# Kernel tuning notes

Hardware: AMD Instinct MI355X
Metric: run time of the kernel (lower is better)

## Reference

```python
import jax, jax.numpy as jnp
import numpy as np

B = 65536
NC = 64          # coarse samples
NF = 128         # fine samples
NEAR, FAR = 2.0, 6.0


def setup_inputs() -> dict:
    key = jax.random.key(0)
    k1, k2, k3, k4, k5, k6 = jax.random.split(key, 6)
    ray_origin = jax.random.normal(k1, (B, 3), dtype=jnp.float32)
    ray_direction = jax.random.normal(k2, (B, 3), dtype=jnp.float32)
    # stratified linspace depths, as in the coarse branch of _sample_points_on_ray
    step = (FAR - NEAR) / (NC - 1)
    coarse_depth_values = jnp.broadcast_to(
        NEAR + jnp.arange(NC, dtype=jnp.float32) * step, (B, NC)
    )
    coarse_weights = jax.random.uniform(k3, (B, NC), dtype=jnp.float32)
    u = jax.random.uniform(k4, (B, NF), dtype=jnp.float32)
    raw_density = jax.random.uniform(k5, (B, NC + NF, 1), dtype=jnp.float32)
    raw_color = jax.random.uniform(k6, (B, NC + NF, 3), dtype=jnp.float32)
    return {
        "ray_origin": ray_origin,
        "ray_direction": ray_direction,
        "coarse_depth_values": coarse_depth_values,
        "coarse_weights": coarse_weights,
        "u": u,
        "raw_density": raw_density,
        "raw_color": raw_color,
    }


def _sample_pdf(bins, weights, u):
    """Inverse-CDF sampling. bins: [B, M+1], weights: [B, M], u: [B, N]."""
    M = weights.shape[1]
    weights = weights + 1e-5
    pdf = weights / jnp.sum(weights, axis=-1, keepdims=True)
    cdf = jnp.cumsum(pdf, axis=-1)                     # [B, M]
    cdf = jnp.concatenate([jnp.zeros_like(cdf[:, :1]), cdf], axis=-1)  # [B, M+1]
    # torch loop `above_inds += (u >= cdf[:, i])` for i in [0, M) ==
    # searchsorted(cdf[:, :M], u, side='right')
    above = jax.vmap(lambda c, uu: jnp.searchsorted(c, uu, side="right"))(
        cdf[:, :M], u
    )                                                  # [B, N], values in [1, M]
    below = jnp.clip(above - 1, 0, None)
    cdf_b = jnp.take_along_axis(cdf, below, axis=-1)
    cdf_a = jnp.take_along_axis(cdf, above, axis=-1)
    bins_b = jnp.take_along_axis(bins, below, axis=-1)
    bins_a = jnp.take_along_axis(bins, above, axis=-1)
    denom = cdf_a - cdf_b
    denom = jnp.where(denom < 1e-5, jnp.ones_like(denom), denom)
    t = (u - cdf_b) / denom
    return bins_b + t * (bins_a - bins_b)


def _composite(raw_density, raw_color, depth_values):
    # distances between consecutive samples, last one = 1e10
    dists = depth_values[..., 1:] - depth_values[..., :-1]
    dists = jnp.concatenate(
        [dists, jnp.full_like(dists[:, :1], 1e10)], axis=-1
    )
    alpha = 1.0 - jnp.exp(-raw_density[..., 0] * dists)          # [B, S]
    T = jnp.cumprod(1.0 - alpha + 1e-10, axis=-1)[:, :-1]
    T = jnp.concatenate([jnp.ones_like(T[:, :1]), T], axis=-1)
    weights = T * alpha                                           # [B, S]
    depth = jnp.sum(weights * depth_values, axis=-1, keepdims=True)
    color = jnp.sum(weights[..., None] * raw_color, axis=-2)      # [B, 3]
    return depth, color, weights


def reference(ray_origin, ray_direction, coarse_depth_values, coarse_weights,
              u, raw_density, raw_color):
    # fine branch of _sample_points_on_ray
    mids = 0.5 * (coarse_depth_values[..., 1:] + coarse_depth_values[..., :-1])
    w = coarse_weights[:, 1:-1]
    fine_depths = _sample_pdf(mids, w, u)                         # [B, NF]
    depth_values = jnp.sort(
        jnp.concatenate([coarse_depth_values, fine_depths], axis=-1), axis=-1
    )                                                             # [B, NC+NF]
    points_on_ray = (
        ray_origin[:, None, :]
        + ray_direction[:, None, :] * depth_values[..., None]
    )                                                             # [B, S, 3]
    depth, color_map, weights = _composite(raw_density, raw_color, depth_values)
    # forward of RenderRay returns the color map; points kept live via dummy use
    del points_on_ray, depth, weights
    return color_map
```

## Files before the change

### kernel.cpp

```cpp
#include <hip/hip_runtime.h>

#define NC 64
#define NF 128
#define NT 192
#define B_TOTAL 65536
#define RPB 4

#define NEAR_F 2.0f
#define STEP_F (4.0f / 63.0f)
#define INV_STEP (63.0f / 4.0f)

__global__ __launch_bounds__(256) void render_ray_kernel(
    const float* __restrict__ cw,
    const float* __restrict__ u_in,
    const float* __restrict__ dens,
    const float* __restrict__ col,
    float* __restrict__ out)
{
    const int wave = threadIdx.x >> 6;
    const int lane = threadIdx.x & 63;
    const int ray  = blockIdx.x * RPB + wave;

    __shared__ float s_cdf [RPB][64];
    __shared__ float s_m   [RPB][200];
    __shared__ int   s_hist[RPB][64];

    const float wraw = cw[(size_t)ray * NC + lane];
    float x = u_in[(size_t)ray * NF + lane];
    float y = u_in[(size_t)ray * NF + 64 + lane];

    const float wv = (lane >= 1 && lane <= 62) ? (wraw + 1e-5f) : 0.0f;
    float ssum = wv;
    #pragma unroll
    for (int off = 32; off; off >>= 1) ssum += __shfl_xor(ssum, off);
    const float pdf = __fdividef(wv, ssum);
    float scan = pdf;
    #pragma unroll
    for (int off = 1; off < 64; off <<= 1) {
        const float t = __shfl_up(scan, off);
        if (lane >= off) scan += t;
    }
    s_cdf[wave][lane]  = scan;
    s_hist[wave][lane] = 0;
    __syncthreads();

    #pragma unroll
    for (int k = 2; k <= 128; k <<= 1) {
        #pragma unroll
        for (int j = k >> 1; j > 0; j >>= 1) {
            if (j == 64) {
                const float mn = fminf(x, y);
                const float mx = fmaxf(x, y);
                x = mn; y = mx;
            } else {
                const bool lower = (lane & j) == 0;
                const bool ascx  = (k >= 128) ? true : ((lane & k) == 0);
                const bool ascy  = (k >= 128) ? true
                                 : ((k == 64) ? false : ((lane & k) == 0));
                const float px = __shfl_xor(x, j);
                const float py = __shfl_xor(y, j);
                x = (ascx == lower) ? fminf(x, px) : fmaxf(x, px);
                y = (ascy == lower) ? fminf(y, py) : fmaxf(y, py);
            }
        }
    }

    const float* __restrict__ cdfp = s_cdf[wave];
    auto sample = [&](float u) -> float {
        int l = 0, h = 62;
        while (l < h) {
            const int mid = (l + h) >> 1;
            if (cdfp[mid] <= u) l = mid + 1; else h = mid;
        }
        const int below = l - 1;
        const float cb = cdfp[below];
        const float ca = cdfp[l];
        float denom = ca - cb;
        if (denom < 1e-5f) denom = 1.0f;
        const float t = __fdividef(u - cb, denom);
        return NEAR_F + ((float)below + 0.5f + t) * STEP_F;
    };

    const float fx = sample(x);
    const float fy = sample(y);
    int gx = (int)floorf((fx - NEAR_F) * INV_STEP) + 1;
    int gy = (int)floorf((fy - NEAR_F) * INV_STEP) + 1;
    gx = min(max(gx, 1), 63);
    gy = min(max(gy, 1), 63);

    s_m[wave][lane + gx]      = fx;
    s_m[wave][lane + 64 + gy] = fy;
    atomicAdd(&s_hist[wave][gx], 1);
    atomicAdd(&s_hist[wave][gy], 1);
    __syncthreads();

    int hsum = s_hist[wave][lane];
    #pragma unroll
    for (int off = 1; off < 64; off <<= 1) {
        const int t = __shfl_up(hsum, off);
        if (lane >= off) hsum += t;
    }
    s_m[wave][lane + hsum] = NEAR_F + (float)lane * STEP_F;
    __syncthreads();

    const float* __restrict__ mp = s_m[wave];
    const int i0 = 3 * lane;
    const float m0 = mp[i0], m1 = mp[i0 + 1], m2 = mp[i0 + 2];
    const float m3 = mp[i0 + 3];
    const float d0 = m1 - m0;
    const float d1 = m2 - m1;
    const float d2 = (lane == 63) ? 1e10f : (m3 - m2);

    const float* __restrict__ dp = dens + (size_t)ray * NT + i0;
    const float a0 = 1.0f - __expf(-dp[0] * d0);
    const float a1 = 1.0f - __expf(-dp[1] * d1);
    const float a2 = 1.0f - __expf(-dp[2] * d2);
    const float f0 = 1.0f - a0 + 1e-10f;
    const float f1 = 1.0f - a1 + 1e-10f;
    const float f2 = 1.0f - a2 + 1e-10f;

    float scanp = f0 * f1 * f2;
    #pragma unroll
    for (int off = 1; off < 64; off <<= 1) {
        const float t = __shfl_up(scanp, off);
        if (lane >= off) scanp *= t;
    }
    float T0 = __shfl_up(scanp, 1);
    if (lane == 0) T0 = 1.0f;
    const float T1 = T0 * f0;
    const float T2 = T1 * f1;

    const float w0 = T0 * (1.0f - f0 + 1e-10f);
    const float w1 = T1 * (1.0f - f1 + 1e-10f);
    const float w2 = T2 * (1.0f - f2 + 1e-10f);

    const float* __restrict__ cp = col + (size_t)ray * NT * 3 + 3 * (size_t)i0;
    float ax = w0 * cp[0] + w1 * cp[3] + w2 * cp[6];
    float ay = w0 * cp[1] + w1 * cp[4] + w2 * cp[7];
    float az = w0 * cp[2] + w1 * cp[5] + w2 * cp[8];

    #pragma unroll
    for (int off = 32; off; off >>= 1) {
        ax += __shfl_xor(ax, off);
        ay += __shfl_xor(ay, off);
        az += __shfl_xor(az, off);
    }
    if (lane == 0) {
        out[(size_t)ray * 3 + 0] = ax;
        out[(size_t)ray * 3 + 1] = ay;
        out[(size_t)ray * 3 + 2] = az;
    }
}

extern "C" void kernel_launch(void* const* d_in, const int* in_sizes, int n_in,
                              void* d_out, int out_size, void* d_ws, size_t ws_size,
                              hipStream_t stream) {
    const float* cwts = (const float*)d_in[3];
    const float* u    = (const float*)d_in[4];
    const float* dens = (const float*)d_in[5];
    const float* col  = (const float*)d_in[6];
    float* out = (float*)d_out;

    dim3 grid(B_TOTAL / RPB);
    dim3 block(256);
    hipLaunchKernelGGL(render_ray_kernel, grid, block, 0, stream,
                       cwts, u, dens, col, out);
}
```

Measured before the change: 290.2 us.

## Prefetch density/color as float4 early, use wave barriers, 4 samples per lane

Issues vectorized float4 loads of density and color at kernel start so their latency overlaps the CDF, sort and search phases. The per-lane work is remapped to 4 samples on 48 lanes so those loads are aligned. Block-wide __syncthreads are replaced with wave barriers, since each wave works only on its own ray's shared memory. The three output components are now written by three lanes instead of one. This raises register pressure from holding the prefetched values and relies on wave-local LDS ordering being correct without a full barrier.

```diff
diff --git a/kernel.cpp b/kernel.cpp
--- a/kernel.cpp
+++ b/kernel.cpp
@@ -29,6 +29,15 @@
     float x = u_in[(size_t)ray * NF + lane];
     float y = u_in[(size_t)ray * NF + 64 + lane];
 
+    float4 dv = make_float4(0.f, 0.f, 0.f, 0.f);
+    float4 c0 = dv, c1 = dv, c2 = dv;
+    const int i0 = 4 * lane;
+    if (lane < 48) {
+        dv = *reinterpret_cast<const float4*>(dens + (size_t)ray * NT + i0);
+        const float4* cp4 = reinterpret_cast<const float4*>(col + (size_t)ray * NT * 3 + 3 * (size_t)i0);
+        c0 = cp4[0]; c1 = cp4[1]; c2 = cp4[2];
+    }
+
     const float wv = (lane >= 1 && lane <= 62) ? (wraw + 1e-5f) : 0.0f;
     float ssum = wv;
     #pragma unroll
@@ -42,7 +51,7 @@
     }
     s_cdf[wave][lane]  = scan;
     s_hist[wave][lane] = 0;
-    __syncthreads();
+    __builtin_amdgcn_wave_barrier();
 
     #pragma unroll
     for (int k = 2; k <= 128; k <<= 1) {
@@ -92,7 +101,7 @@
     s_m[wave][lane + 64 + gy] = fy;
     atomicAdd(&s_hist[wave][gx], 1);
     atomicAdd(&s_hist[wave][gy], 1);
-    __syncthreads();
+    __builtin_amdgcn_wave_barrier();
 
     int hsum = s_hist[wave][lane];
     #pragma unroll
@@ -101,25 +110,24 @@
         if (lane >= off) hsum += t;
     }
     s_m[wave][lane + hsum] = NEAR_F + (float)lane * STEP_F;
-    __syncthreads();
+    __builtin_amdgcn_wave_barrier();
 
     const float* __restrict__ mp = s_m[wave];
-    const int i0 = 3 * lane;
-    const float m0 = mp[i0], m1 = mp[i0 + 1], m2 = mp[i0 + 2];
-    const float m3 = mp[i0 + 3];
-    const float d0 = m1 - m0;
-    const float d1 = m2 - m1;
-    const float d2 = (lane == 63) ? 1e10f : (m3 - m2);
+    float f0 = 1.0f, f1 = 1.0f, f2 = 1.0f, f3 = 1.0f;
+    if (lane < 48) {
+        const float m0 = mp[i0], m1 = mp[i0 + 1], m2 = mp[i0 + 2], m3 = mp[i0 + 3];
+        const float m4 = mp[(lane == 47) ? 191 : (i0 + 4)];
+        const float d0 = m1 - m0;
+        const float d1 = m2 - m1;
+        const float d2 = m3 - m2;
+        const float d3 = (lane == 47) ? 1e10f : (m4 - m3);
+        f0 = 1.0f - (1.0f - __expf(-dv.x * d0)) + 1e-10f;
+        f1 = 1.0f - (1.0f - __expf(-dv.y * d1)) + 1e-10f;
+        f2 = 1.0f - (1.0f - __expf(-dv.z * d2)) + 1e-10f;
+        f3 = 1.0f - (1.0f - __expf(-dv.w * d3)) + 1e-10f;
+    }
 
-    const float* __restrict__ dp = dens + (size_t)ray * NT + i0;
-    const float a0 = 1.0f - __expf(-dp[0] * d0);
-    const float a1 = 1.0f - __expf(-dp[1] * d1);
-    const float a2 = 1.0f - __expf(-dp[2] * d2);
-    const float f0 = 1.0f - a0 + 1e-10f;
-    const float f1 = 1.0f - a1 + 1e-10f;
-    const float f2 = 1.0f - a2 + 1e-10f;
-
-    float scanp = f0 * f1 * f2;
+    float scanp = f0 * f1 * f2 * f3;
     #pragma unroll
     for (int off = 1; off < 64; off <<= 1) {
         const float t = __shfl_up(scanp, off);
@@ -129,15 +137,18 @@
     if (lane == 0) T0 = 1.0f;
     const float T1 = T0 * f0;
     const float T2 = T1 * f1;
+    const float T3 = T2 * f2;
 
-    const float w0 = T0 * (1.0f - f0 + 1e-10f);
-    const float w1 = T1 * (1.0f - f1 + 1e-10f);
-    const float w2 = T2 * (1.0f - f2 + 1e-10f);
-
-    const float* __restrict__ cp = col + (size_t)ray * NT * 3 + 3 * (size_t)i0;
-    float ax = w0 * cp[0] + w1 * cp[3] + w2 * cp[6];
-    float ay = w0 * cp[1] + w1 * cp[4] + w2 * cp[7];
-    float az = w0 * cp[2] + w1 * cp[5] + w2 * cp[8];
+    float ax = 0.f, ay = 0.f, az = 0.f;
+    if (lane < 48) {
+        const float w0 = T0 * (1.0f - f0 + 1e-10f);
+        const float w1 = T1 * (1.0f - f1 + 1e-10f);
+        const float w2 = T2 * (1.0f - f2 + 1e-10f);
+        const float w3 = T3 * (1.0f - f3 + 1e-10f);
+        ax = w0 * c0.x + w1 * c0.w + w2 * c1.z + w3 * c2.y;
+        ay = w0 * c0.y + w1 * c1.x + w2 * c1.w + w3 * c2.z;
+        az = w0 * c0.z + w1 * c1.y + w2 * c2.x + w3 * c2.w;
+    }
 
     #pragma unroll
     for (int off = 32; off; off >>= 1) {
@@ -145,10 +156,9 @@
         ay += __shfl_xor(ay, off);
         az += __shfl_xor(az, off);
     }
-    if (lane == 0) {
-        out[(size_t)ray * 3 + 0] = ax;
-        out[(size_t)ray * 3 + 1] = ay;
-        out[(size_t)ray * 3 + 2] = az;
+    if (lane < 3) {
+        const float v = (lane == 0) ? ax : ((lane == 1) ? ay : az);
+        out[(size_t)ray * 3 + lane] = v;
     }
 }
 
```

New measurement: 298.3 us. 2.8% more time.
